# Kernel tuning notes

Measured on AMD Instinct MI355X. Metric: run time of the kernel, lower is better.

Reference implementation:

```python
import jax, jax.numpy as jnp
import numpy as np

DIM = 256
NH = 8
HD = DIM // NH
SCALE = HD ** -0.5


def setup_inputs() -> dict:
    key = jax.random.key(0)
    ks = jax.random.split(key, 11)
    Bn, Mh, Mw, C = 2048, 8, 8, DIM
    x = jax.random.normal(ks[0], (Bn, Mh, Mw, C), dtype=jnp.float32)
    y = jax.random.normal(ks[1], (Bn, Mh, Mw, C), dtype=jnp.float32)
    z = jax.random.normal(ks[2], (Bn, Mh, Mw, C), dtype=jnp.float32)
    s = 0.02
    q_w = jax.random.normal(ks[3], (C, C), dtype=jnp.float32) * s
    q_b = jnp.zeros((C,), dtype=jnp.float32)
    k_w = jax.random.normal(ks[4], (C, C), dtype=jnp.float32) * s
    k_b = jnp.zeros((C,), dtype=jnp.float32)
    v_w = jax.random.normal(ks[5], (C, C), dtype=jnp.float32) * s
    v_b = jnp.zeros((C,), dtype=jnp.float32)
    proj_w = jax.random.normal(ks[6], (C, C), dtype=jnp.float32) * s
    proj_b = jnp.zeros((C,), dtype=jnp.float32)
    return {"x": x, "y": y, "z": z, "q_w": q_w, "q_b": q_b, "k_w": k_w,
            "k_b": k_b, "v_w": v_w, "v_b": v_b, "proj_w": proj_w, "proj_b": proj_b}


def softmax_plus_one(a):
    m = jnp.max(a, axis=-1, keepdims=True)
    e = jnp.exp(a - m)
    return e / (jnp.sum(e, axis=-1, keepdims=True) + 1.0)


def reference(x, y, z, q_w, q_b, k_w, k_b, v_w, v_b, proj_w, proj_b):
    Bn, Mh, Mw, C = x.shape
    L = Mh * Mw
    xf = x.reshape(Bn, L, C)
    yf = y.reshape(Bn, L, C)
    # z is rearranged but unused in the original forward

    def heads(t, w, b):
        # torch Linear: t @ w.T + b, then split heads -> (Bn, Nh, L, HD)
        p = t @ w.T + b
        return p.reshape(Bn, L, NH, HD).transpose(0, 2, 1, 3)

    q1 = heads(yf, q_w, q_b) * SCALE
    k1 = heads(xf, k_w, k_b)
    v1 = heads(xf, v_w, v_b)

    attn = jnp.einsum('bnqd,bnkd->bnqk', q1, k1)  # (Bn, Nh, L, L)
    attn = softmax_plus_one(attn)
    y1 = jnp.einsum('bnqk,bnkd->bnqd', attn, v1)  # (Bn, Nh, L, HD)
    y1 = y1.transpose(0, 2, 1, 3).reshape(Bn, Mh, Mw, C)

    out = y + y1
    out = out @ proj_w.T + proj_b
    return out
```

## Files before the change

### kernel.cpp

```cpp
#include <hip/hip_runtime.h>

typedef __bf16 bf16x8 __attribute__((ext_vector_type(8)));
typedef __bf16 bf16x4 __attribute__((ext_vector_type(4)));
typedef short  s16x4  __attribute__((ext_vector_type(4)));
typedef float  f32x4  __attribute__((ext_vector_type(4)));
typedef unsigned int u32x4 __attribute__((ext_vector_type(4)));
typedef unsigned int u32x2 __attribute__((ext_vector_type(2)));
typedef unsigned int u32;
typedef unsigned short u16;

#define DEVI static __device__ __forceinline__

static constexpr float KSCALE = 0.17677669529663687f;

DEVI u32 pk2(float a, float b){
  u16 ha = __builtin_bit_cast(u16, (__bf16)a);
  u16 hb = __builtin_bit_cast(u16, (__bf16)b);
  return (u32)ha | ((u32)hb << 16);
}
DEVI float bfl(u32 bits16){
  union { u32 i; float f; } v; v.i = bits16 << 16; return v.f;
}
DEVI u32x2 pkfrag(f32x4 v){ u32x2 o; o[0]=pk2(v[0],v[1]); o[1]=pk2(v[2],v[3]); return o; }
DEVI bf16x8 ld16(const void* p){ return __builtin_bit_cast(bf16x8, *(const u32x4*)p); }
DEVI f32x4 mfma16(bf16x8 a, bf16x8 b, f32x4 c){
  return __builtin_amdgcn_mfma_f32_16x16x32_bf16(a, b, c, 0, 0, 0);
}
DEVI f32x4 mfma1616(u32x2 a, u32x2 b, f32x4 c){
#if __has_builtin(__builtin_amdgcn_mfma_f32_16x16x16_bf16)
  return __builtin_amdgcn_mfma_f32_16x16x16_bf16(
      __builtin_bit_cast(bf16x4, a), __builtin_bit_cast(bf16x4, b), c, 0, 0, 0);
#elif __has_builtin(__builtin_amdgcn_mfma_f32_16x16x16bf16_1k)
  return __builtin_amdgcn_mfma_f32_16x16x16bf16_1k(
      __builtin_bit_cast(s16x4, a), __builtin_bit_cast(s16x4, b), c, 0, 0, 0);
#else
  asm("v_mfma_f32_16x16x16_bf16 %0, %1, %2, %0" : "+v"(c) : "v"(a), "v"(b));
  return c;
#endif
}

template<bool BW>
DEVI bf16x8 loadw(const u16* wbp, const float* wfp){
  if constexpr (BW){
    return ld16(wbp);
  } else {
    f32x4 a = *(const f32x4*)wfp;
    f32x4 b = *(const f32x4*)(wfp + 4);
    u32x4 pc; pc[0]=pk2(a[0],a[1]); pc[1]=pk2(a[2],a[3]); pc[2]=pk2(b[0],b[1]); pc[3]=pk2(b[2],b[3]);
    return __builtin_bit_cast(bf16x8, pc);
  }
}

__global__ void prep_w(const float* __restrict__ qw, const float* __restrict__ kw,
                       const float* __restrict__ vw, const float* __restrict__ pw,
                       u16* __restrict__ dst){
  int blk = blockIdx.x;
  int l   = threadIdx.x;
  int M = blk >> 7, R = (blk >> 3) & 15, kk = blk & 7;
  const float* W = (M==0) ? qw : (M==1) ? kw : (M==2) ? vw : pw;
  const float* src = W + (R*16 + (l&15))*256 + kk*32 + (l>>4)*8;
  f32x4 a  = *(const f32x4*)src;
  f32x4 b2 = *(const f32x4*)(src + 4);
  u32x4 pc; pc[0]=pk2(a[0],a[1]); pc[1]=pk2(a[2],a[3]); pc[2]=pk2(b2[0],b2[1]); pc[3]=pk2(b2[2],b2[3]);
  *(u32x4*)(dst + (size_t)blk*512 + l*8) = pc;
}

DEVI const u16* wfrag(const u16* wb, int M, int R, int kk, int l){
  return wb + ((((M<<4) + R)<<3) + kk)*512 + l*8;
}

template<bool BW>
__global__ __launch_bounds__(256, 2)
void fused_ca(const float* __restrict__ x, const float* __restrict__ y,
              const u16* __restrict__ wb,
              const float* __restrict__ qwf, const float* __restrict__ kwf,
              const float* __restrict__ vwf, const float* __restrict__ pwf,
              const float* __restrict__ qb, const float* __restrict__ kb,
              const float* __restrict__ vb, const float* __restrict__ pb,
              float* __restrict__ out)
{
  extern __shared__ char smem[];
  const int b  = blockIdx.x;
  const int t  = threadIdx.x;
  const int w  = t >> 6;
  const int l  = t & 63;
  const int lo = l & 15;
  const int g  = l >> 4;
  const u32 swr = (u32)(lo & 7) << 4;

  char* r1 = smem;
  char* Xs = smem + 32768;

  const float* yb = y + (size_t)b * 16384;
  const float* xb = x + (size_t)b * 16384;

  #pragma unroll
  for (int j = 0; j < 16; ++j){
    int idx = t + 256*j;
    int row = idx >> 6;
    int c0  = (idx & 63) * 4;
    f32x4 v = *(const f32x4*)(yb + row*256 + c0);
    u32x2 o; o[0] = pk2(v[0], v[1]); o[1] = pk2(v[2], v[3]);
    *(u32x2*)(r1 + row*512 + ((u32)(c0*2) ^ ((u32)(row&7) << 4))) = o;
  }
  f32x4 xr[8];
  #pragma unroll
  for (int j = 0; j < 8; ++j){
    int idx = t + 256*j;
    xr[j] = *(const f32x4*)(xb + (idx>>6)*256 + (idx & 63)*4);
  }
  __syncthreads();

  u32x2 aqpk[2][8];
  #pragma unroll
  for (int hl = 0; hl < 2; ++hl){
    const int cb = w*64 + hl*32;
    const int Rb = w*4 + hl*2;
    f32x4 aq[2][4] = {};
    #pragma unroll
    for (int kk = 0; kk < 8; ++kk){
      bf16x8 A[2], Bf[4];
      #pragma unroll
      for (int m = 0; m < 2; ++m){
        int off = (cb + 16*m + lo)*256 + kk*32 + 8*g;
        A[m] = loadw<BW>(wfrag(wb, 0, Rb + m, kk, l), qwf + off);
      }
      #pragma unroll
      for (int n = 0; n < 4; ++n)
        Bf[n] = ld16(r1 + (16*n+lo)*512 + ((u32)(kk*64 + 16*g) ^ swr));
      #pragma unroll
      for (int m = 0; m < 2; ++m)
        #pragma unroll
        for (int n = 0; n < 4; ++n)
          aq[m][n] = mfma16(A[m], Bf[n], aq[m][n]);
    }
    #pragma unroll
    for (int m = 0; m < 2; ++m){
      f32x4 bias = *(const f32x4*)(qb + cb + 16*m + 4*g);
      #pragma unroll
      for (int n = 0; n < 4; ++n){
        f32x4 v; 
        #pragma unroll
        for (int r = 0; r < 4; ++r) v[r] = (aq[m][n][r] + bias[r]) * KSCALE;
        aqpk[hl][m*4+n] = pkfrag(v);
      }
    }
    if (hl == 0){
      #pragma unroll
      for (int j = 0; j < 8; ++j){
        int idx = t + 256*j;
        int row = idx >> 6;
        int c0  = (idx & 63) * 4;
        u32x2 o; o[0] = pk2(xr[j][0], xr[j][1]); o[1] = pk2(xr[j][2], xr[j][3]);
        *(u32x2*)(Xs + row*512 + ((u32)(c0*2) ^ ((u32)(row&7) << 4))) = o;
      }
      #pragma unroll
      for (int j = 0; j < 8; ++j){
        int idx = t + 256*(j+8);
        xr[j] = *(const f32x4*)(xb + (idx>>6)*256 + (idx & 63)*4);
      }
    }
  }
  #pragma unroll
  for (int j = 0; j < 8; ++j){
    int idx = t + 256*(j+8);
    int row = idx >> 6;
    int c0  = (idx & 63) * 4;
    u32x2 o; o[0] = pk2(xr[j][0], xr[j][1]); o[1] = pk2(xr[j][2], xr[j][3]);
    *(u32x2*)(Xs + row*512 + ((u32)(c0*2) ^ ((u32)(row&7) << 4))) = o;
  }
  __syncthreads();

  #pragma unroll
  for (int hl = 0; hl < 2; ++hl){
    const int cb = w*64 + hl*32;
    const int Rb = w*4 + hl*2;

    f32x4 ak[2][4] = {};
    f32x4 av[4][2] = {};
    #pragma unroll
    for (int kk = 0; kk < 8; ++kk){
      bf16x8 WA[2], WB2[2], XF[4];
      #pragma unroll
      for (int m = 0; m < 2; ++m){
        int off = (cb + 16*m + lo)*256 + kk*32 + 8*g;
        WA[m] = loadw<BW>(wfrag(wb, 1, Rb + m, kk, l), kwf + off);
      }
      #pragma unroll
      for (int n = 0; n < 2; ++n){
        int off = (cb + 16*n + lo)*256 + kk*32 + 8*g;
        WB2[n] = loadw<BW>(wfrag(wb, 2, Rb + n, kk, l), vwf + off);
      }
      #pragma unroll
      for (int f = 0; f < 4; ++f)
        XF[f] = ld16(Xs + (16*f+lo)*512 + ((u32)(kk*64 + 16*g) ^ swr));
      #pragma unroll
      for (int f = 0; f < 4; ++f){
        #pragma unroll
        for (int m = 0; m < 2; ++m)
          ak[m][f] = mfma16(WA[m], XF[f], ak[m][f]);
        #pragma unroll
        for (int n = 0; n < 2; ++n)
          av[f][n] = mfma16(XF[f], WB2[n], av[f][n]);
      }
    }
    u32x2 akpk[8], avpk[8];
    #pragma unroll
    for (int m = 0; m < 2; ++m){
      f32x4 bias = *(const f32x4*)(kb + cb + 16*m + 4*g);
      #pragma unroll
      for (int f = 0; f < 4; ++f){
        f32x4 v;
        #pragma unroll
        for (int r = 0; r < 4; ++r) v[r] = ak[m][f][r] + bias[r];
        akpk[m*4+f] = pkfrag(v);
      }
    }
    #pragma unroll
    for (int n = 0; n < 2; ++n){
      float bias = vb[cb + 16*n + lo];
      #pragma unroll
      for (int f = 0; f < 4; ++f){
        f32x4 v;
        #pragma unroll
        for (int r = 0; r < 4; ++r) v[r] = av[f][n][r] + bias;
        avpk[f*2+n] = pkfrag(v);
      }
    }

    f32x4 y1h[2][4] = {};
    #pragma unroll
    for (int n = 0; n < 4; ++n){
      f32x4 s4[4];
      #pragma unroll
      for (int f = 0; f < 4; ++f){
        f32x4 acc = {};
        acc = mfma1616(akpk[0*4+f], aqpk[hl][0*4+n], acc);
        acc = mfma1616(akpk[1*4+f], aqpk[hl][1*4+n], acc);
        s4[f] = acc;
      }
      float mx = s4[0][0];
      #pragma unroll
      for (int f = 0; f < 4; ++f)
        #pragma unroll
        for (int r = 0; r < 4; ++r)
          mx = fmaxf(mx, s4[f][r]);
      mx = fmaxf(mx, __shfl_xor(mx, 16));
      mx = fmaxf(mx, __shfl_xor(mx, 32));
      float sum = 0.f;
      #pragma unroll
      for (int f = 0; f < 4; ++f)
        #pragma unroll
        for (int r = 0; r < 4; ++r){
          float e = __expf(s4[f][r] - mx);
          s4[f][r] = e; sum += e;
        }
      sum += __shfl_xor(sum, 16);
      sum += __shfl_xor(sum, 32);
      float rin = 1.0f / (sum + 1.0f);
      u32x2 spk[4];
      #pragma unroll
      for (int f = 0; f < 4; ++f){
        f32x4 v;
        #pragma unroll
        for (int r = 0; r < 4; ++r) v[r] = s4[f][r] * rin;
        spk[f] = pkfrag(v);
      }
      #pragma unroll
      for (int md = 0; md < 2; ++md)
        #pragma unroll
        for (int f = 0; f < 4; ++f)
          y1h[md][n] = mfma1616(avpk[f*2+md], spk[f], y1h[md][n]);
    }

    #pragma unroll
    for (int md = 0; md < 2; ++md)
      #pragma unroll
      for (int n = 0; n < 4; ++n){
        int c0 = cb + 16*md + 4*g;
        char* p = r1 + (16*n+lo)*512 + ((u32)(c0*2) ^ swr);
        u32x2 old = *(const u32x2*)p;
        f32x4 a = y1h[md][n];
        float o0 = bfl(old[0] & 0xffffu) + a[0];
        float o1 = bfl(old[0] >> 16)     + a[1];
        float o2 = bfl(old[1] & 0xffffu) + a[2];
        float o3 = bfl(old[1] >> 16)     + a[3];
        u32x2 nw; nw[0] = pk2(o0, o1); nw[1] = pk2(o2, o3);
        *(u32x2*)p = nw;
      }
  }

  __syncthreads();

  f32x4 ap[4][4] = {};
  #pragma unroll
  for (int kk = 0; kk < 8; ++kk){
    bf16x8 Af[4], Bp[4];
    #pragma unroll
    for (int m = 0; m < 4; ++m)
      Af[m] = ld16(r1 + (16*m+lo)*512 + ((u32)(kk*64 + 16*g) ^ swr));
    #pragma unroll
    for (int n = 0; n < 4; ++n){
      int off = (w*64 + 16*n + lo)*256 + kk*32 + 8*g;
      Bp[n] = loadw<BW>(wfrag(wb, 3, w*4 + n, kk, l), pwf + off);
    }
    #pragma unroll
    for (int m = 0; m < 4; ++m)
      #pragma unroll
      for (int n = 0; n < 4; ++n)
        ap[m][n] = mfma16(Af[m], Bp[n], ap[m][n]);
  }

  float pbv[4];
  #pragma unroll
  for (int n = 0; n < 4; ++n) pbv[n] = pb[w*64 + 16*n + lo];
  #pragma unroll
  for (int m = 0; m < 4; ++m)
    #pragma unroll
    for (int n = 0; n < 4; ++n)
      #pragma unroll
      for (int r = 0; r < 4; ++r)
        ap[m][n][r] += pbv[n];

  float* ob = out + (size_t)b * 16384;
  #pragma unroll
  for (int half = 0; half < 2; ++half){
    __syncthreads();
    #pragma unroll
    for (int mm = 0; mm < 2; ++mm)
      #pragma unroll
      for (int n = 0; n < 4; ++n){
        int col = w*64 + 16*n + lo;
        #pragma unroll
        for (int r = 0; r < 4; ++r){
          int row = mm*16 + 4*g + r;
          u32 byteoff = ((u32)(row*1024 + col*4)) ^ ((u32)(row & 4) << 4);
          *(float*)(r1 + byteoff) = ap[half*2 + mm][n][r];
        }
      }
    __syncthreads();
    #pragma unroll
    for (int i = 0; i < 8; ++i){
      int id  = i*256 + t;
      int row = id >> 6;
      int cc  = id & 63;
      u32 byteoff = (u32)(row*1024) + ((u32)(cc ^ (row & 4)) << 4);
      f32x4 v = *(const f32x4*)(r1 + byteoff);
      *(f32x4*)(ob + (half*32 + row)*256 + cc*4) = v;
    }
  }
}

extern "C" void kernel_launch(void* const* d_in, const int* in_sizes, int n_in,
                              void* d_out, int out_size, void* d_ws, size_t ws_size,
                              hipStream_t stream) {
  (void)n_in; (void)out_size;
  const float* x  = (const float*)d_in[0];
  const float* y  = (const float*)d_in[1];
  const float* qw = (const float*)d_in[3];
  const float* qb = (const float*)d_in[4];
  const float* kw = (const float*)d_in[5];
  const float* kb = (const float*)d_in[6];
  const float* vw = (const float*)d_in[7];
  const float* vb = (const float*)d_in[8];
  const float* pw = (const float*)d_in[9];
  const float* pb = (const float*)d_in[10];
  float* out = (float*)d_out;
  const int Bn = in_sizes[0] / 16384;

  const bool useWs = ws_size >= (size_t)524288;
  if (useWs){
    u16* wsb = (u16*)d_ws;
    prep_w<<<512, 64, 0, stream>>>(qw, kw, vw, pw, wsb);
    (void)hipFuncSetAttribute(reinterpret_cast<const void*>(&fused_ca<true>),
                              hipFuncAttributeMaxDynamicSharedMemorySize, 65536);
    fused_ca<true><<<Bn, 256, 65536, stream>>>(x, y, wsb, qw, kw, vw, pw,
                                               qb, kb, vb, pb, out);
  } else {
    (void)hipFuncSetAttribute(reinterpret_cast<const void*>(&fused_ca<false>),
                              hipFuncAttributeMaxDynamicSharedMemorySize, 65536);
    fused_ca<false><<<Bn, 256, 65536, stream>>>(x, y, (const u16*)d_ws, qw, kw, vw, pw,
                                                qb, kb, vb, pb, out);
  }
}
```

Measured before the change: 173.0 us.

## Halve X staging buffer and compute K/V in two row halves to cut LDS

X is now staged in shared memory in two 32-row halves instead of all 64 rows. K and V projections are computed per half for both head-pairs, with the packed results held in registers across both halves. Dynamic LDS drops from 64KB to 48KB, which may allow more blocks per CU on a 160KB-LDS device. The cost is an extra barrier pair and the K/V weight fragments being reloaded for each half, plus more live registers (akpk/avpk for both head-pairs).

```diff
diff --git a/kernel.cpp b/kernel.cpp
--- a/kernel.cpp
+++ b/kernel.cpp
@@ -69,6 +69,13 @@
   return wb + ((((M<<4) + R)<<3) + kk)*512 + l*8;
 }
 
+DEVI void stw(char* T, int idx, f32x4 v){
+  int row = idx >> 6;
+  int c0  = (idx & 63) * 4;
+  u32x2 o; o[0] = pk2(v[0], v[1]); o[1] = pk2(v[2], v[3]);
+  *(u32x2*)(T + row*512 + ((u32)(c0*2) ^ ((u32)(row&7) << 4))) = o;
+}
+
 template<bool BW>
 __global__ __launch_bounds__(256, 2)
 void fused_ca(const float* __restrict__ x, const float* __restrict__ y,
@@ -80,6 +87,8 @@
               float* __restrict__ out)
 {
   extern __shared__ char smem[];
+  char* r1 = smem;
+  char* Xs = smem + 32768;
   const int b  = blockIdx.x;
   const int t  = threadIdx.x;
   const int w  = t >> 6;
@@ -88,26 +97,24 @@
   const int g  = l >> 4;
   const u32 swr = (u32)(lo & 7) << 4;
 
-  char* r1 = smem;
-  char* Xs = smem + 32768;
-
   const float* yb = y + (size_t)b * 16384;
   const float* xb = x + (size_t)b * 16384;
 
-  #pragma unroll
-  for (int j = 0; j < 16; ++j){
-    int idx = t + 256*j;
-    int row = idx >> 6;
-    int c0  = (idx & 63) * 4;
-    f32x4 v = *(const f32x4*)(yb + row*256 + c0);
-    u32x2 o; o[0] = pk2(v[0], v[1]); o[1] = pk2(v[2], v[3]);
-    *(u32x2*)(r1 + row*512 + ((u32)(c0*2) ^ ((u32)(row&7) << 4))) = o;
-  }
-  f32x4 xr[8];
-  #pragma unroll
-  for (int j = 0; j < 8; ++j){
-    int idx = t + 256*j;
-    xr[j] = *(const f32x4*)(xb + (idx>>6)*256 + (idx & 63)*4);
+  {
+    f32x4 x0r[8];
+    #pragma unroll
+    for (int j = 0; j < 8; ++j){
+      int idx = t + 256*j;
+      x0r[j] = *(const f32x4*)(xb + (idx>>6)*256 + (idx&63)*4);
+    }
+    #pragma unroll
+    for (int j = 0; j < 16; ++j){
+      int idx = t + 256*j;
+      f32x4 v = *(const f32x4*)(yb + (idx>>6)*256 + (idx&63)*4);
+      stw(r1, idx, v);
+    }
+    #pragma unroll
+    for (int j = 0; j < 8; ++j) stw(Xs, t + 256*j, x0r[j]);
   }
   __syncthreads();
 
@@ -139,95 +146,155 @@
       f32x4 bias = *(const f32x4*)(qb + cb + 16*m + 4*g);
       #pragma unroll
       for (int n = 0; n < 4; ++n){
-        f32x4 v; 
+        f32x4 v;
         #pragma unroll
         for (int r = 0; r < 4; ++r) v[r] = (aq[m][n][r] + bias[r]) * KSCALE;
         aqpk[hl][m*4+n] = pkfrag(v);
       }
     }
-    if (hl == 0){
-      #pragma unroll
-      for (int j = 0; j < 8; ++j){
-        int idx = t + 256*j;
-        int row = idx >> 6;
-        int c0  = (idx & 63) * 4;
-        u32x2 o; o[0] = pk2(xr[j][0], xr[j][1]); o[1] = pk2(xr[j][2], xr[j][3]);
-        *(u32x2*)(Xs + row*512 + ((u32)(c0*2) ^ ((u32)(row&7) << 4))) = o;
-      }
-      #pragma unroll
-      for (int j = 0; j < 8; ++j){
-        int idx = t + 256*(j+8);
-        xr[j] = *(const f32x4*)(xb + (idx>>6)*256 + (idx & 63)*4);
-      }
-    }
-  }
+  }
+
+  u32x2 akpk[2][8], avpk[2][8];
+  f32x4 x1r[8];
   #pragma unroll
   for (int j = 0; j < 8; ++j){
-    int idx = t + 256*(j+8);
-    int row = idx >> 6;
-    int c0  = (idx & 63) * 4;
-    u32x2 o; o[0] = pk2(xr[j][0], xr[j][1]); o[1] = pk2(xr[j][2], xr[j][3]);
-    *(u32x2*)(Xs + row*512 + ((u32)(c0*2) ^ ((u32)(row&7) << 4))) = o;
+    int idx = 2048 + t + 256*j;
+    x1r[j] = *(const f32x4*)(xb + (idx>>6)*256 + (idx&63)*4);
+  }
+  {
+    f32x4 ak[2][2][2] = {};
+    f32x4 av[2][2][2] = {};
+    #pragma unroll
+    for (int kk = 0; kk < 8; ++kk){
+      bf16x8 XF[2];
+      #pragma unroll
+      for (int fl = 0; fl < 2; ++fl)
+        XF[fl] = ld16(Xs + (16*fl+lo)*512 + ((u32)(kk*64 + 16*g) ^ swr));
+      #pragma unroll
+      for (int hl = 0; hl < 2; ++hl){
+        const int cb = w*64 + hl*32;
+        const int Rb = w*4 + hl*2;
+        bf16x8 WA[2], WB2[2];
+        #pragma unroll
+        for (int m = 0; m < 2; ++m){
+          int off = (cb + 16*m + lo)*256 + kk*32 + 8*g;
+          WA[m] = loadw<BW>(wfrag(wb, 1, Rb + m, kk, l), kwf + off);
+        }
+        #pragma unroll
+        for (int n = 0; n < 2; ++n){
+          int off = (cb + 16*n + lo)*256 + kk*32 + 8*g;
+          WB2[n] = loadw<BW>(wfrag(wb, 2, Rb + n, kk, l), vwf + off);
+        }
+        #pragma unroll
+        for (int fl = 0; fl < 2; ++fl){
+          #pragma unroll
+          for (int m = 0; m < 2; ++m)
+            ak[hl][m][fl] = mfma16(WA[m], XF[fl], ak[hl][m][fl]);
+          #pragma unroll
+          for (int n = 0; n < 2; ++n)
+            av[hl][fl][n] = mfma16(XF[fl], WB2[n], av[hl][fl][n]);
+        }
+      }
+    }
+    #pragma unroll
+    for (int hl = 0; hl < 2; ++hl){
+      const int cb = w*64 + hl*32;
+      #pragma unroll
+      for (int m = 0; m < 2; ++m){
+        f32x4 bias = *(const f32x4*)(kb + cb + 16*m + 4*g);
+        #pragma unroll
+        for (int fl = 0; fl < 2; ++fl){
+          f32x4 v;
+          #pragma unroll
+          for (int r = 0; r < 4; ++r) v[r] = ak[hl][m][fl][r] + bias[r];
+          akpk[hl][m*4+fl] = pkfrag(v);
+        }
+      }
+      #pragma unroll
+      for (int n = 0; n < 2; ++n){
+        float bias = vb[cb + 16*n + lo];
+        #pragma unroll
+        for (int fl = 0; fl < 2; ++fl){
+          f32x4 v;
+          #pragma unroll
+          for (int r = 0; r < 4; ++r) v[r] = av[hl][fl][n][r] + bias;
+          avpk[hl][fl*2+n] = pkfrag(v);
+        }
+      }
+    }
   }
   __syncthreads();
+
+  #pragma unroll
+  for (int j = 0; j < 8; ++j) stw(Xs, t + 256*j, x1r[j]);
+  __syncthreads();
+
+  {
+    f32x4 ak[2][2][2] = {};
+    f32x4 av[2][2][2] = {};
+    #pragma unroll
+    for (int kk = 0; kk < 8; ++kk){
+      bf16x8 XF[2];
+      #pragma unroll
+      for (int fl = 0; fl < 2; ++fl)
+        XF[fl] = ld16(Xs + (16*fl+lo)*512 + ((u32)(kk*64 + 16*g) ^ swr));
+      #pragma unroll
+      for (int hl = 0; hl < 2; ++hl){
+        const int cb = w*64 + hl*32;
+        const int Rb = w*4 + hl*2;
+        bf16x8 WA[2], WB2[2];
+        #pragma unroll
+        for (int m = 0; m < 2; ++m){
+          int off = (cb + 16*m + lo)*256 + kk*32 + 8*g;
+          WA[m] = loadw<BW>(wfrag(wb, 1, Rb + m, kk, l), kwf + off);
+        }
+        #pragma unroll
+        for (int n = 0; n < 2; ++n){
+          int off = (cb + 16*n + lo)*256 + kk*32 + 8*g;
+          WB2[n] = loadw<BW>(wfrag(wb, 2, Rb + n, kk, l), vwf + off);
+        }
+        #pragma unroll
+        for (int fl = 0; fl < 2; ++fl){
+          #pragma unroll
+          for (int m = 0; m < 2; ++m)
+            ak[hl][m][fl] = mfma16(WA[m], XF[fl], ak[hl][m][fl]);
+          #pragma unroll
+          for (int n = 0; n < 2; ++n)
+            av[hl][fl][n] = mfma16(XF[fl], WB2[n], av[hl][fl][n]);
+        }
+      }
+    }
+    #pragma unroll
+    for (int hl = 0; hl < 2; ++hl){
+      const int cb = w*64 + hl*32;
+      #pragma unroll
+      for (int m = 0; m < 2; ++m){
+        f32x4 bias = *(const f32x4*)(kb + cb + 16*m + 4*g);
+        #pragma unroll
+        for (int fl = 0; fl < 2; ++fl){
+          f32x4 v;
+          #pragma unroll
+          for (int r = 0; r < 4; ++r) v[r] = ak[hl][m][fl][r] + bias[r];
+          akpk[hl][m*4+2+fl] = pkfrag(v);
+        }
+      }
+      #pragma unroll
+      for (int n = 0; n < 2; ++n){
+        float bias = vb[cb + 16*n + lo];
+        #pragma unroll
+        for (int fl = 0; fl < 2; ++fl){
+          f32x4 v;
+          #pragma unroll
+          for (int r = 0; r < 4; ++r) v[r] = av[hl][fl][n][r] + bias;
+          avpk[hl][(2+fl)*2+n] = pkfrag(v);
+        }
+      }
+    }
+  }
 
   #pragma unroll
   for (int hl = 0; hl < 2; ++hl){
     const int cb = w*64 + hl*32;
-    const int Rb = w*4 + hl*2;
-
-    f32x4 ak[2][4] = {};
-    f32x4 av[4][2] = {};
-    #pragma unroll
-    for (int kk = 0; kk < 8; ++kk){
-      bf16x8 WA[2], WB2[2], XF[4];
-      #pragma unroll
-      for (int m = 0; m < 2; ++m){
-        int off = (cb + 16*m + lo)*256 + kk*32 + 8*g;
-        WA[m] = loadw<BW>(wfrag(wb, 1, Rb + m, kk, l), kwf + off);
-      }
-      #pragma unroll
-      for (int n = 0; n < 2; ++n){
-        int off = (cb + 16*n + lo)*256 + kk*32 + 8*g;
-        WB2[n] = loadw<BW>(wfrag(wb, 2, Rb + n, kk, l), vwf + off);
-      }
-      #pragma unroll
-      for (int f = 0; f < 4; ++f)
-        XF[f] = ld16(Xs + (16*f+lo)*512 + ((u32)(kk*64 + 16*g) ^ swr));
-      #pragma unroll
-      for (int f = 0; f < 4; ++f){
-        #pragma unroll
-        for (int m = 0; m < 2; ++m)
-          ak[m][f] = mfma16(WA[m], XF[f], ak[m][f]);
-        #pragma unroll
-        for (int n = 0; n < 2; ++n)
-          av[f][n] = mfma16(XF[f], WB2[n], av[f][n]);
-      }
-    }
-    u32x2 akpk[8], avpk[8];
-    #pragma unroll
-    for (int m = 0; m < 2; ++m){
-      f32x4 bias = *(const f32x4*)(kb + cb + 16*m + 4*g);
-      #pragma unroll
-      for (int f = 0; f < 4; ++f){
-        f32x4 v;
-        #pragma unroll
-        for (int r = 0; r < 4; ++r) v[r] = ak[m][f][r] + bias[r];
-        akpk[m*4+f] = pkfrag(v);
-      }
-    }
-    #pragma unroll
-    for (int n = 0; n < 2; ++n){
-      float bias = vb[cb + 16*n + lo];
-      #pragma unroll
-      for (int f = 0; f < 4; ++f){
-        f32x4 v;
-        #pragma unroll
-        for (int r = 0; r < 4; ++r) v[r] = av[f][n][r] + bias;
-        avpk[f*2+n] = pkfrag(v);
-      }
-    }
-
     f32x4 y1h[2][4] = {};
     #pragma unroll
     for (int n = 0; n < 4; ++n){
@@ -235,8 +302,8 @@
       #pragma unroll
       for (int f = 0; f < 4; ++f){
         f32x4 acc = {};
-        acc = mfma1616(akpk[0*4+f], aqpk[hl][0*4+n], acc);
-        acc = mfma1616(akpk[1*4+f], aqpk[hl][1*4+n], acc);
+        acc = mfma1616(akpk[hl][0*4+f], aqpk[hl][0*4+n], acc);
+        acc = mfma1616(akpk[hl][1*4+f], aqpk[hl][1*4+n], acc);
         s4[f] = acc;
       }
       float mx = s4[0][0];
@@ -270,7 +337,7 @@
       for (int md = 0; md < 2; ++md)
         #pragma unroll
         for (int f = 0; f < 4; ++f)
-          y1h[md][n] = mfma1616(avpk[f*2+md], spk[f], y1h[md][n]);
+          y1h[md][n] = mfma1616(avpk[hl][f*2+md], spk[f], y1h[md][n]);
     }
 
     #pragma unroll
@@ -289,7 +356,6 @@
         *(u32x2*)p = nw;
       }
   }
-
   __syncthreads();
 
   f32x4 ap[4][4] = {};
@@ -373,13 +439,13 @@
     u16* wsb = (u16*)d_ws;
     prep_w<<<512, 64, 0, stream>>>(qw, kw, vw, pw, wsb);
     (void)hipFuncSetAttribute(reinterpret_cast<const void*>(&fused_ca<true>),
-                              hipFuncAttributeMaxDynamicSharedMemorySize, 65536);
-    fused_ca<true><<<Bn, 256, 65536, stream>>>(x, y, wsb, qw, kw, vw, pw,
+                              hipFuncAttributeMaxDynamicSharedMemorySize, 49152);
+    fused_ca<true><<<Bn, 256, 49152, stream>>>(x, y, wsb, qw, kw, vw, pw,
                                                qb, kb, vb, pb, out);
   } else {
     (void)hipFuncSetAttribute(reinterpret_cast<const void*>(&fused_ca<false>),
-                              hipFuncAttributeMaxDynamicSharedMemorySize, 65536);
-    fused_ca<false><<<Bn, 256, 65536, stream>>>(x, y, (const u16*)d_ws, qw, kw, vw, pw,
+                              hipFuncAttributeMaxDynamicSharedMemorySize, 49152);
+    fused_ca<false><<<Bn, 256, 49152, stream>>>(x, y, (const u16*)d_ws, qw, kw, vw, pw,
                                                 qb, kb, vb, pb, out);
   }
 }
```

Result: slower. 189.6 us (+9.6%).
